# Kernel optimization log

Hardware: AMD Instinct MI355X
Metric: run time of the kernel (lower is better)

The kernel has to match this reference:

```python
import jax, jax.numpy as jnp
import numpy as np

B, D, H, L, T = 4096, 1024, 2048, 256, 8
STD = 0.02


def setup_inputs() -> dict:
    key = jax.random.key(0)
    ks = jax.random.split(key, 24)
    n = lambda k, shp: (jax.random.normal(k, shp, dtype=jnp.float32) * STD)
    inp = {
        "x": jax.random.uniform(ks[0], (B, D), dtype=jnp.float32),
        "task": jax.random.randint(ks[1], (B,), 0, T),
        "eps": jax.random.normal(ks[2], (B, L), dtype=jnp.float32),
        # per-task encoder stacks: in->H->H->H->2L
        "enc_W1": n(ks[3], (T, D, H)), "enc_b1": jnp.zeros((T, H)),
        "enc_W2": n(ks[4], (T, H, H)), "enc_b2": jnp.zeros((T, H)),
        "enc_W3": n(ks[5], (T, H, H)), "enc_b3": jnp.zeros((T, H)),
        "enc_W4": n(ks[6], (T, H, 2 * L)), "enc_b4": jnp.zeros((T, 2 * L)),
        # shared decoder (BayesianLinear means): L->H->H
        "ds_W1": n(ks[7], (L, H)), "ds_b1": jnp.zeros((H,)),
        "ds_W2": n(ks[8], (H, H)), "ds_b2": jnp.zeros((H,)),
        # per-task decoder heads: H->H->D with Sigmoid
        "hd_W1": n(ks[9], (T, H, H)), "hd_b1": jnp.zeros((T, H)),
        "hd_W2": n(ks[10], (T, H, D)), "hd_b2": jnp.zeros((T, D)),
    }
    return inp


def reference(x, task, eps,
              enc_W1, enc_b1, enc_W2, enc_b2, enc_W3, enc_b3, enc_W4, enc_b4,
              ds_W1, ds_b1, ds_W2, ds_b2,
              hd_W1, hd_b1, hd_W2, hd_b2):
    ntasks = enc_W1.shape[0]
    onehot = jax.nn.one_hot(task, ntasks, dtype=x.dtype)  # [B, T], the task==idx mask

    # ---- encode: run every task's encoder on the full batch, mask-sum ----
    def enc_one(W1, b1, W2, b2, W3, b3, W4, b4):
        h = jax.nn.relu(x @ W1 + b1)
        h = jax.nn.relu(h @ W2 + b2)
        h = jax.nn.relu(h @ W3 + b3)
        return h @ W4 + b4  # [B, 2L]

    enc_all = jax.vmap(enc_one)(enc_W1, enc_b1, enc_W2, enc_b2,
                                enc_W3, enc_b3, enc_W4, enc_b4)  # [T, B, 2L]
    scat = jnp.einsum('tbd,bt->bd', enc_all, onehot)  # [B, 2L]
    latent = scat.shape[1] // 2
    mu, log_sigma = scat[:, :latent], scat[:, latent:]
    z = mu + jnp.exp(log_sigma) * eps  # reparameterization

    # ---- decode: shared trunk, then every head masked ----
    h = jax.nn.relu(z @ ds_W1 + ds_b1)
    h = jax.nn.relu(h @ ds_W2 + ds_b2)  # [B, H]

    def head_one(W1, b1, W2, b2):
        g = jax.nn.relu(h @ W1 + b1)
        return jax.nn.sigmoid(g @ W2 + b2)  # [B, D]

    heads_all = jax.vmap(head_one)(hd_W1, hd_b1, hd_W2, hd_b2)  # [T, B, D]
    return jnp.einsum('tbd,bt->bd', heads_all, onehot)  # [B, D]
```

## Files before the change

kernel.cpp:

```cpp
#include <hip/hip_runtime.h>
#include <hip/hip_bf16.h>

#define T_TASKS 8
#define B_ROWS 4096
#define PADROWS 4224
#define BM 128
#define BK 32
#define MAXTILES 40

typedef __attribute__((ext_vector_type(4))) float f32x4;
typedef __attribute__((ext_vector_type(8))) short bf16x8;

#define GLOAD_LDS16(g, l) __builtin_amdgcn_global_load_lds( \
    (const __attribute__((address_space(1))) void*)(g), \
    (__attribute__((address_space(3))) void*)(l), 16, 0, 0)

struct TP { const float* src; unsigned short* dst; int K; int N; int ntiles; };

__device__ __forceinline__ unsigned short f32_to_bf16(float f) {
    union { float f; unsigned int u; } v; v.f = f;
    unsigned int r = v.u + 0x7FFF + ((v.u >> 16) & 1);
    return (unsigned short)(r >> 16);
}

__global__ void setup_kernel(const int* __restrict__ task, int* __restrict__ perm,
                             int* __restrict__ offs, int* __restrict__ table) {
    __shared__ int cnt[T_TASKS];
    __shared__ int cur[T_TASKS];
    int tid = threadIdx.x;
    if (tid < T_TASKS) cnt[tid] = 0;
    __syncthreads();
    for (int b = tid; b < B_ROWS; b += blockDim.x)
        atomicAdd(&cnt[task[b]], 1);
    __syncthreads();
    if (tid == 0) {
        int o = 0;
        for (int t = 0; t < T_TASKS; ++t) { offs[t] = o; cur[t] = o; o += cnt[t]; }
        offs[T_TASKS] = o;
        int s = 0;
        for (int t = 0; t < T_TASKS; ++t) {
            int nt = (cnt[t] + BM - 1) / BM;
            for (int j = 0; j < nt; ++j) table[s++] = (t << 16) | j;
        }
        for (; s < MAXTILES; ++s) table[s] = -1;
    }
    __syncthreads();
    for (int b = tid; b < B_ROWS; b += blockDim.x) {
        int t = task[b];
        int pos = atomicAdd(&cur[t], 1);
        perm[pos] = b;
    }
}

__global__ void permute_cast_kernel(const float* __restrict__ x, const int* __restrict__ perm,
                                    unsigned short* __restrict__ xp) {
    int rowp = blockIdx.x;
    int src = perm[rowp];
    const float4* xin = reinterpret_cast<const float4*>(x + (size_t)src * 1024);
    unsigned short* dst = xp + (size_t)rowp * 1024;
    int c4 = threadIdx.x;
    float4 v = xin[c4];
    ushort4 o;
    o.x = f32_to_bf16(v.x); o.y = f32_to_bf16(v.y);
    o.z = f32_to_bf16(v.z); o.w = f32_to_bf16(v.w);
    *reinterpret_cast<ushort4*>(dst + c4 * 4) = o;
}

__global__ void vae_kernel(const float* __restrict__ scat, const float* __restrict__ eps,
                           const int* __restrict__ perm, unsigned short* __restrict__ z) {
    int rowp = blockIdx.x;
    int c = threadIdx.x;
    int src = perm[rowp];
    float mu = scat[(size_t)rowp * 512 + c];
    float ls = scat[(size_t)rowp * 512 + 256 + c];
    float e  = eps[(size_t)src * 256 + c];
    z[(size_t)rowp * 256 + c] = f32_to_bf16(mu + __expf(ls) * e);
}

__global__ __launch_bounds__(256)
void transpose_cast_kernel(const float* __restrict__ W, unsigned short* __restrict__ Wt,
                           int K, int N) {
    const size_t toff = (size_t)blockIdx.z * K * N;
    const float* Ws = W + toff;
    unsigned short* Wd = Wt + toff;
    const int k0 = blockIdx.x * 64;
    const int n0 = blockIdx.y * 64;
    __shared__ unsigned short Tt[64 * 64];
    const int tid = threadIdx.x;
    const int n = tid & 63;
    const int kq = tid >> 6;
    #pragma unroll
    for (int i = 0; i < 4; ++i) {
        int kk = kq * 16 + i * 4;
        const float* p = Ws + (size_t)(k0 + kk) * N + n0 + n;
        float v0 = p[0];
        float v1 = p[(size_t)N];
        float v2 = p[(size_t)2 * N];
        float v3 = p[(size_t)3 * N];
        unsigned int lo = (unsigned int)f32_to_bf16(v0) | ((unsigned int)f32_to_bf16(v1) << 16);
        unsigned int hi = (unsigned int)f32_to_bf16(v2) | ((unsigned int)f32_to_bf16(v3) << 16);
        int c = (kk >> 2) ^ (n & 15);
        *reinterpret_cast<uint2*>(Tt + n * 64 + c * 4) = make_uint2(lo, hi);
    }
    __syncthreads();
    #pragma unroll
    for (int it = 0; it < 2; ++it) {
        int c  = it * 256 + tid;
        int nn = c >> 3;
        int cg = c & 7;
        int c1 = (cg * 2) ^ (nn & 15);
        int c2 = (cg * 2 + 1) ^ (nn & 15);
        uint2 a = *reinterpret_cast<const uint2*>(Tt + nn * 64 + c1 * 4);
        uint2 b = *reinterpret_cast<const uint2*>(Tt + nn * 64 + c2 * 4);
        uint4 o = make_uint4(a.x, a.y, b.x, b.y);
        *reinterpret_cast<uint4*>(Wd + (size_t)(n0 + nn) * K + k0 + cg * 8) = o;
    }
}

template<int MODE, int BN>
__global__ __launch_bounds__(256, (BN == 64 ? 6 : 4))
void gemm12_kernel(const unsigned short* __restrict__ A,
                   const unsigned short* __restrict__ Wt,
                   const float* __restrict__ bias, void* __restrict__ dst,
                   const int* __restrict__ offs, const int* __restrict__ table,
                   const int* __restrict__ perm,
                   int K, int N, int ldd, int Btot, int GX, TP tpa, TP tpb)
{
    constexpr int NR = BN / 32;
    __shared__ unsigned short As[2][BM * BK];
    __shared__ unsigned short Bs[2][BN * BK];

    const int bxh = blockIdx.x;
    const int tid = threadIdx.x;

    if (bxh >= GX) {
        int tile = (bxh - GX) * gridDim.y + blockIdx.y;
        const float* src; unsigned short* dstp; int tK, tN;
        if (tile < tpa.ntiles) { src = tpa.src; dstp = tpa.dst; tK = tpa.K; tN = tpa.N; }
        else {
            tile -= tpa.ntiles;
            if (tile >= tpb.ntiles) return;
            src = tpb.src; dstp = tpb.dst; tK = tpb.K; tN = tpb.N;
        }
        int tk = tK >> 6, tn = tN >> 6;
        int z = tile / (tk * tn);
        int r = tile % (tk * tn);
        int k0 = (r % tk) * 64, n0 = (r / tk) * 64;
        const size_t toff = (size_t)z * tK * tN;
        const float* Ws = src + toff;
        unsigned short* Wd = dstp + toff;
        unsigned short* Tt = &As[0][0];
        const int n = tid & 63;
        const int kq = tid >> 6;
        #pragma unroll
        for (int i = 0; i < 4; ++i) {
            int kk = kq * 16 + i * 4;
            const float* p = Ws + (size_t)(k0 + kk) * tN + n0 + n;
            float v0 = p[0];
            float v1 = p[(size_t)tN];
            float v2 = p[(size_t)2 * tN];
            float v3 = p[(size_t)3 * tN];
            unsigned int lo = (unsigned int)f32_to_bf16(v0) | ((unsigned int)f32_to_bf16(v1) << 16);
            unsigned int hi = (unsigned int)f32_to_bf16(v2) | ((unsigned int)f32_to_bf16(v3) << 16);
            int c = (kk >> 2) ^ (n & 15);
            *reinterpret_cast<uint2*>(Tt + n * 64 + c * 4) = make_uint2(lo, hi);
        }
        __syncthreads();
        #pragma unroll
        for (int it = 0; it < 2; ++it) {
            int c  = it * 256 + tid;
            int nn = c >> 3;
            int cg = c & 7;
            int c1 = (cg * 2) ^ (nn & 15);
            int c2 = (cg * 2 + 1) ^ (nn & 15);
            uint2 a = *reinterpret_cast<const uint2*>(Tt + nn * 64 + c1 * 4);
            uint2 b = *reinterpret_cast<const uint2*>(Tt + nn * 64 + c2 * 4);
            uint4 o = make_uint4(a.x, a.y, b.x, b.y);
            *reinterpret_cast<uint4*>(Wd + (size_t)(n0 + nn) * tK + k0 + cg * 8) = o;
        }
        return;
    }

    int bx = (bxh & 7) * (GX >> 3) + (bxh >> 3);

    int t, mtile, off, cnt;
    if (table != nullptr) {
        int v = table[bx];
        if (v < 0) return;
        t = v >> 16; mtile = v & 0xFFFF;
        off = offs[t]; cnt = offs[t + 1] - off;
    } else {
        t = 0; mtile = bx; off = 0; cnt = Btot;
    }
    const int n0 = blockIdx.y * BN;

    const int lane = tid & 63;
    const int wave = tid >> 6;
    const int wr = wave >> 1, wc = wave & 1;

    const int rl   = lane >> 2;
    const int csrc = ((lane & 3) ^ ((rl >> 1) & 3)) * 8;
    const unsigned short* Ab = A + ((size_t)(off + mtile * BM + rl)) * K + csrc;
    const unsigned short* Bb = Wt + ((size_t)t * N + n0 + rl) * K + csrc;

    auto stage = [&](int buf, int k0) {
        #pragma unroll
        for (int jj = 0; jj < 2; ++jj) {
            int j = wave * 2 + jj;
            GLOAD_LDS16(Ab + (size_t)(j * 16) * K + k0, &As[buf][j * 512]);
        }
        #pragma unroll
        for (int jb = 0; jb < BN / 64; ++jb) {
            int j = wave * (BN / 64) + jb;
            GLOAD_LDS16(Bb + (size_t)(j * 16) * K + k0, &Bs[buf][j * 512]);
        }
    };

    f32x4 acc[4][NR];
    #pragma unroll
    for (int m = 0; m < 4; ++m)
        #pragma unroll
        for (int n = 0; n < NR; ++n)
            acc[m][n] = (f32x4){0.f, 0.f, 0.f, 0.f};

    auto compute = [&](int buf) {
        bf16x8 af[4], bfr[NR];
        #pragma unroll
        for (int m = 0; m < 4; ++m) {
            int rf = wr * 64 + m * 16 + (lane & 15);
            af[m] = *reinterpret_cast<const bf16x8*>(
                &As[buf][rf * 32 + (((lane >> 4) ^ ((rf >> 1) & 3)) * 8)]);
        }
        #pragma unroll
        for (int n = 0; n < NR; ++n) {
            int nf = wc * (BN / 2) + n * 16 + (lane & 15);
            bfr[n] = *reinterpret_cast<const bf16x8*>(
                &Bs[buf][nf * 32 + (((lane >> 4) ^ ((nf >> 1) & 3)) * 8)]);
        }
        #pragma unroll
        for (int m = 0; m < 4; ++m)
            #pragma unroll
            for (int n = 0; n < NR; ++n)
                acc[m][n] = __builtin_amdgcn_mfma_f32_16x16x32_bf16(af[m], bfr[n], acc[m][n], 0, 0, 0);
    };

    const int nsteps = K / BK;
    stage(0, 0);
    __syncthreads();
    int cur = 0;
    for (int s = 0; s < nsteps; ++s) {
        if (s + 1 < nsteps) stage(cur ^ 1, (s + 1) * BK);
        compute(cur);
        __syncthreads();
        cur ^= 1;
    }

    const float* bt = bias + (size_t)t * N;
    #pragma unroll
    for (int n = 0; n < NR; ++n) {
        int col = n0 + wc * (BN / 2) + n * 16 + (lane & 15);
        float bv = bt[col];
        #pragma unroll
        for (int m = 0; m < 4; ++m) {
            int rbase = mtile * BM + wr * 64 + m * 16 + ((lane >> 4) << 2);
            #pragma unroll
            for (int j = 0; j < 4; ++j) {
                int local = rbase + j;
                if (local >= cnt) continue;
                float v = acc[m][n][j] + bv;
                if (MODE == 0) {
                    ((unsigned short*)dst)[(size_t)(off + local) * ldd + col] =
                        f32_to_bf16(fmaxf(v, 0.f));
                } else if (MODE == 1) {
                    ((float*)dst)[(size_t)(off + local) * ldd + col] = v;
                } else {
                    int grow = perm[off + local];
                    ((float*)dst)[(size_t)grow * ldd + col] = 1.f / (1.f + __expf(-v));
                }
            }
        }
    }
}

extern "C" void kernel_launch(void* const* d_in, const int* in_sizes, int n_in,
                              void* d_out, int out_size, void* d_ws, size_t ws_size,
                              hipStream_t stream) {
    const float* x      = (const float*)d_in[0];
    const int*   task   = (const int*)d_in[1];
    const float* eps    = (const float*)d_in[2];
    const float* enc_W1 = (const float*)d_in[3];
    const float* enc_b1 = (const float*)d_in[4];
    const float* enc_W2 = (const float*)d_in[5];
    const float* enc_b2 = (const float*)d_in[6];
    const float* enc_W3 = (const float*)d_in[7];
    const float* enc_b3 = (const float*)d_in[8];
    const float* enc_W4 = (const float*)d_in[9];
    const float* enc_b4 = (const float*)d_in[10];
    const float* ds_W1  = (const float*)d_in[11];
    const float* ds_b1  = (const float*)d_in[12];
    const float* ds_W2  = (const float*)d_in[13];
    const float* ds_b2  = (const float*)d_in[14];
    const float* hd_W1  = (const float*)d_in[15];
    const float* hd_b1  = (const float*)d_in[16];
    const float* hd_W2  = (const float*)d_in[17];
    const float* hd_b2  = (const float*)d_in[18];
    float* out = (float*)d_out;

    char* ws = (char*)d_ws;
    int* perm  = (int*)ws;
    int* offs  = (int*)(ws + 16384);
    int* table = (int*)(ws + 16384 + 256);
    char* p = ws + 32768;
    unsigned short* xp = (unsigned short*)p; p += (size_t)PADROWS * 1024 * 2;
    unsigned short* h1 = (unsigned short*)p; p += (size_t)PADROWS * 2048 * 2;
    unsigned short* h2 = (unsigned short*)p; p += (size_t)PADROWS * 2048 * 2;
    unsigned short* zb = (unsigned short*)p; p += (size_t)PADROWS * 256 * 2;
    unsigned short* tw1  = (unsigned short*)p; p += (size_t)8 * 2048 * 1024 * 2;
    unsigned short* tw2  = (unsigned short*)p; p += (size_t)8 * 2048 * 2048 * 2;
    unsigned short* tw3  = (unsigned short*)p; p += (size_t)8 * 2048 * 2048 * 2;
    unsigned short* tw4  = (unsigned short*)p; p += (size_t)8 * 512 * 2048 * 2;
    unsigned short* tds1 = (unsigned short*)p; p += (size_t)2048 * 256 * 2;
    unsigned short* tds2 = (unsigned short*)p; p += (size_t)2048 * 2048 * 2;
    unsigned short* thd1 = (unsigned short*)p; p += (size_t)8 * 2048 * 2048 * 2;
    unsigned short* thd2 = (unsigned short*)p; p += (size_t)8 * 1024 * 2048 * 2;
    float* scat = out;

    const TP tnone = { nullptr, nullptr, 64, 64, 0 };
    const TP tpW2  = { enc_W2, tw2, 2048, 2048, 8192 };
    const TP tpW3  = { enc_W3, tw3, 2048, 2048, 8192 };
    const TP tpW4  = { enc_W4, tw4, 2048,  512, 2048 };
    const TP tpDS1 = { ds_W1, tds1,  256, 2048,  128 };
    const TP tpDS2 = { ds_W2, tds2, 2048, 2048, 1024 };
    const TP tpHD1 = { hd_W1, thd1, 2048, 2048, 8192 };
    const TP tpHD2 = { hd_W2, thd2, 2048, 1024, 4096 };

    setup_kernel<<<1, 1024, 0, stream>>>(task, perm, offs, table);
    permute_cast_kernel<<<B_ROWS, 256, 0, stream>>>(x, perm, xp);

    transpose_cast_kernel<<<dim3(16, 32, 8), 256, 0, stream>>>(enc_W1, tw1, 1024, 2048);

    gemm12_kernel<0, 128><<<dim3(552, 16), 256, 0, stream>>>(xp, tw1, enc_b1, h1, offs, table, nullptr, 1024, 2048, 2048, B_ROWS, MAXTILES, tpW2, tnone);
    gemm12_kernel<0, 128><<<dim3(552, 16), 256, 0, stream>>>(h1, tw2, enc_b2, h2, offs, table, nullptr, 2048, 2048, 2048, B_ROWS, MAXTILES, tpW3, tnone);
    gemm12_kernel<0, 128><<<dim3(176, 16), 256, 0, stream>>>(h2, tw3, enc_b3, h1, offs, table, nullptr, 2048, 2048, 2048, B_ROWS, MAXTILES, tpW4, tpDS1);
    gemm12_kernel<1, 64><<<dim3(168, 8), 256, 0, stream>>>(h1, tw4, enc_b4, scat, offs, table, nullptr, 2048, 512, 512, B_ROWS, MAXTILES, tpDS2, tnone);

    vae_kernel<<<B_ROWS, 256, 0, stream>>>(scat, eps, perm, zb);

    gemm12_kernel<0, 128><<<dim3(544, 16), 256, 0, stream>>>(zb, tds1, ds_b1, h2, nullptr, nullptr, nullptr, 256, 2048, 2048, B_ROWS, 32, tpHD1, tnone);
    gemm12_kernel<0, 128><<<dim3(288, 16), 256, 0, stream>>>(h2, tds2, ds_b2, h1, nullptr, nullptr, nullptr, 2048, 2048, 2048, B_ROWS, 32, tpHD2, tnone);

    gemm12_kernel<0, 128><<<dim3(MAXTILES, 16), 256, 0, stream>>>(h1, thd1, hd_b1, h2, offs, table, nullptr, 2048, 2048, 2048, B_ROWS, MAXTILES, tnone, tnone);
    gemm12_kernel<2, 64><<<dim3(MAXTILES, 16), 256, 0, stream>>>(h2, thd2, hd_b2, out, offs, table, perm, 2048, 1024, 1024, B_ROWS, MAXTILES, tnone, tnone);
}
```

Measured before the change: 618.0 us.

## Add 256x256 8-wave ping-pong GEMM kernel for large H×H layers

After: 726.8 us. +17.6%, slower.

```diff
diff --git a/kernel.cpp b/kernel.cpp
--- a/kernel.cpp
+++ b/kernel.cpp
@@ -3,10 +3,9 @@
 
 #define T_TASKS 8
 #define B_ROWS 4096
-#define PADROWS 4224
-#define BM 128
-#define BK 32
-#define MAXTILES 40
+#define PADROWS 4352
+#define MAXT128 40
+#define MAXT256 24
 
 typedef __attribute__((ext_vector_type(4))) float f32x4;
 typedef __attribute__((ext_vector_type(8))) short bf16x8;
@@ -14,6 +13,9 @@
 #define GLOAD_LDS16(g, l) __builtin_amdgcn_global_load_lds( \
     (const __attribute__((address_space(1))) void*)(g), \
     (__attribute__((address_space(3))) void*)(l), 16, 0, 0)
+
+#define WAITV2() asm volatile("s_waitcnt vmcnt(2)" ::: "memory")
+#define PBAR()   asm volatile("s_barrier" ::: "memory")
 
 struct TP { const float* src; unsigned short* dst; int K; int N; int ntiles; };
 
@@ -24,7 +26,8 @@
 }
 
 __global__ void setup_kernel(const int* __restrict__ task, int* __restrict__ perm,
-                             int* __restrict__ offs, int* __restrict__ table) {
+                             int* __restrict__ offs, int* __restrict__ table128,
+                             int* __restrict__ table256) {
     __shared__ int cnt[T_TASKS];
     __shared__ int cur[T_TASKS];
     int tid = threadIdx.x;
@@ -39,10 +42,16 @@
         offs[T_TASKS] = o;
         int s = 0;
         for (int t = 0; t < T_TASKS; ++t) {
-            int nt = (cnt[t] + BM - 1) / BM;
-            for (int j = 0; j < nt; ++j) table[s++] = (t << 16) | j;
-        }
-        for (; s < MAXTILES; ++s) table[s] = -1;
+            int nt = (cnt[t] + 127) >> 7;
+            for (int j = 0; j < nt; ++j) table128[s++] = (t << 16) | j;
+        }
+        for (; s < MAXT128; ++s) table128[s] = -1;
+        s = 0;
+        for (int t = 0; t < T_TASKS; ++t) {
+            int nt = (cnt[t] + 255) >> 8;
+            for (int j = 0; j < nt; ++j) table256[s++] = (t << 16) | j;
+        }
+        for (; s < MAXT256; ++s) table256[s] = -1;
     }
     __syncthreads();
     for (int b = tid; b < B_ROWS; b += blockDim.x) {
@@ -117,6 +126,191 @@
     }
 }
 
+template<int MODE>
+__global__ __launch_bounds__(512, 2)
+void gemm8p_kernel(const unsigned short* __restrict__ A,
+                   const unsigned short* __restrict__ Wt,
+                   const float* __restrict__ bias, void* __restrict__ dst,
+                   const int* __restrict__ offs, const int* __restrict__ table,
+                   const int* __restrict__ perm,
+                   int K, int N, int ldd, int Btot, int GX, TP tpa, TP tpb)
+{
+    __shared__ unsigned short As_[2][256 * 64];
+    __shared__ unsigned short Bs_[2][256 * 64];
+
+    const int bxh = blockIdx.x;
+    const int tid = threadIdx.x;
+
+    if (bxh >= GX) {
+        int half = tid >> 8;
+        int ltid = tid & 255;
+        int tile = ((bxh - GX) * gridDim.y + blockIdx.y) * 2 + half;
+        unsigned short* Tt = &As_[0][0] + half * 4096;
+        const float* src = nullptr; unsigned short* dstp = nullptr; int tK = 64, tN = 64;
+        bool act = true;
+        if (tile < tpa.ntiles) { src = tpa.src; dstp = tpa.dst; tK = tpa.K; tN = tpa.N; }
+        else {
+            tile -= tpa.ntiles;
+            if (tile >= tpb.ntiles) act = false;
+            else { src = tpb.src; dstp = tpb.dst; tK = tpb.K; tN = tpb.N; }
+        }
+        int k0 = 0, n0 = 0; size_t toff = 0;
+        if (act) {
+            int tk = tK >> 6, tn = tN >> 6;
+            int z = tile / (tk * tn);
+            int r = tile % (tk * tn);
+            k0 = (r % tk) * 64; n0 = (r / tk) * 64;
+            toff = (size_t)z * tK * tN;
+        }
+        const int n = ltid & 63;
+        const int kq = ltid >> 6;
+        if (act) {
+            const float* Ws = src + toff;
+            #pragma unroll
+            for (int i = 0; i < 4; ++i) {
+                int kk = kq * 16 + i * 4;
+                const float* p = Ws + (size_t)(k0 + kk) * tN + n0 + n;
+                float v0 = p[0];
+                float v1 = p[(size_t)tN];
+                float v2 = p[(size_t)2 * tN];
+                float v3 = p[(size_t)3 * tN];
+                unsigned int lo = (unsigned int)f32_to_bf16(v0) | ((unsigned int)f32_to_bf16(v1) << 16);
+                unsigned int hi = (unsigned int)f32_to_bf16(v2) | ((unsigned int)f32_to_bf16(v3) << 16);
+                int c = (kk >> 2) ^ (n & 15);
+                *reinterpret_cast<uint2*>(Tt + n * 64 + c * 4) = make_uint2(lo, hi);
+            }
+        }
+        __syncthreads();
+        if (act) {
+            unsigned short* Wd = dstp + toff;
+            #pragma unroll
+            for (int it = 0; it < 2; ++it) {
+                int c  = it * 256 + ltid;
+                int nn = c >> 3;
+                int cg = c & 7;
+                int c1 = (cg * 2) ^ (nn & 15);
+                int c2 = (cg * 2 + 1) ^ (nn & 15);
+                uint2 a = *reinterpret_cast<const uint2*>(Tt + nn * 64 + c1 * 4);
+                uint2 b = *reinterpret_cast<const uint2*>(Tt + nn * 64 + c2 * 4);
+                uint4 o = make_uint4(a.x, a.y, b.x, b.y);
+                *reinterpret_cast<uint4*>(Wd + (size_t)(n0 + nn) * tK + k0 + cg * 8) = o;
+            }
+        }
+        return;
+    }
+
+    int bx = (bxh & 7) * (GX >> 3) + (bxh >> 3);
+
+    int t, mtile, off, cnt;
+    if (table != nullptr) {
+        int v = table[bx];
+        if (v < 0) return;
+        t = v >> 16; mtile = v & 0xFFFF;
+        off = offs[t]; cnt = offs[t + 1] - off;
+    } else {
+        t = 0; mtile = bx; off = 0; cnt = Btot;
+    }
+    const int n0 = blockIdx.y * 256;
+
+    const int lane = tid & 63;
+    const int wave = tid >> 6;
+    const int wm = wave >> 2;
+    const int wn = wave & 3;
+
+    const int aRow  = lane >> 3;
+    const int aSlot = ((lane & 7) ^ aRow) * 8;
+    const unsigned short* Ab = A + ((size_t)(off + mtile * 256 + aRow)) * K + aSlot;
+    const unsigned short* Bb = Wt + ((size_t)t * N + n0 + aRow) * K + aSlot;
+
+    const int nt = K >> 6;
+
+    auto stA = [&](int c, int h, int kt) {
+        int k0 = (kt < nt ? kt : nt - 1) << 6;
+        #pragma unroll
+        for (int j = 0; j < 2; ++j) {
+            int r0 = h * 128 + (wave * 2 + j) * 8;
+            GLOAD_LDS16(Ab + (size_t)r0 * K + k0, &As_[c][r0 * 64]);
+        }
+    };
+    auto stB = [&](int c, int h, int kt) {
+        int k0 = (kt < nt ? kt : nt - 1) << 6;
+        #pragma unroll
+        for (int j = 0; j < 2; ++j) {
+            int r0 = h * 128 + (wave * 2 + j) * 8;
+            GLOAD_LDS16(Bb + (size_t)r0 * K + k0, &Bs_[c][r0 * 64]);
+        }
+    };
+
+    f32x4 acc[8][4];
+    #pragma unroll
+    for (int m = 0; m < 8; ++m)
+        #pragma unroll
+        for (int n = 0; n < 4; ++n)
+            acc[m][n] = (f32x4){0.f, 0.f, 0.f, 0.f};
+
+    auto comp = [&](int c, int mg, int kf) {
+        bf16x8 af[4], bfr[4];
+        #pragma unroll
+        for (int m = 0; m < 4; ++m) {
+            int rf = wm * 128 + (mg * 4 + m) * 16 + (lane & 15);
+            af[m] = *reinterpret_cast<const bf16x8*>(
+                &As_[c][rf * 64 + (((kf * 4 + (lane >> 4)) ^ (rf & 7)) * 8)]);
+        }
+        #pragma unroll
+        for (int n = 0; n < 4; ++n) {
+            int nf = wn * 64 + n * 16 + (lane & 15);
+            bfr[n] = *reinterpret_cast<const bf16x8*>(
+                &Bs_[c][nf * 64 + (((kf * 4 + (lane >> 4)) ^ (nf & 7)) * 8)]);
+        }
+        #pragma unroll
+        for (int m = 0; m < 4; ++m)
+            #pragma unroll
+            for (int n = 0; n < 4; ++n)
+                acc[mg * 4 + m][n] =
+                    __builtin_amdgcn_mfma_f32_16x16x32_bf16(af[m], bfr[n], acc[mg * 4 + m][n], 0, 0, 0);
+    };
+
+    stB(0, 0, 0); stB(0, 1, 0); stA(0, 0, 0); stA(0, 1, 0);
+
+    for (int i = 0; i < (nt >> 1); ++i) {
+        int T1 = 2 * i + 1, T2 = 2 * i + 2;
+        stB(1, 0, T1); WAITV2(); PBAR(); comp(0, 0, 0); PBAR();
+        stB(1, 1, T1);           PBAR(); comp(0, 1, 0); PBAR();
+        stA(1, 0, T1);           PBAR(); comp(0, 0, 1); PBAR();
+        stA(1, 1, T1);           PBAR(); comp(0, 1, 1); PBAR();
+        stB(0, 0, T2); WAITV2(); PBAR(); comp(1, 0, 0); PBAR();
+        stB(0, 1, T2);           PBAR(); comp(1, 1, 0); PBAR();
+        stA(0, 0, T2);           PBAR(); comp(1, 0, 1); PBAR();
+        stA(0, 1, T2);           PBAR(); comp(1, 1, 1); PBAR();
+    }
+
+    const float* bt = bias + (size_t)t * N;
+    #pragma unroll
+    for (int mi = 0; mi < 8; ++mi) {
+        int rbase = mtile * 256 + wm * 128 + mi * 16 + ((lane >> 4) << 2);
+        #pragma unroll
+        for (int n = 0; n < 4; ++n) {
+            int col = n0 + wn * 64 + n * 16 + (lane & 15);
+            float bv = bt[col];
+            #pragma unroll
+            for (int j = 0; j < 4; ++j) {
+                int local = rbase + j;
+                if (local >= cnt) continue;
+                float v = acc[mi][n][j] + bv;
+                if (MODE == 0) {
+                    ((unsigned short*)dst)[(size_t)(off + local) * ldd + col] =
+                        f32_to_bf16(fmaxf(v, 0.f));
+                } else if (MODE == 1) {
+                    ((float*)dst)[(size_t)(off + local) * ldd + col] = v;
+                } else {
+                    int grow = perm[off + local];
+                    ((float*)dst)[(size_t)grow * ldd + col] = 1.f / (1.f + __expf(-v));
+                }
+            }
+        }
+    }
+}
+
 template<int MODE, int BN>
 __global__ __launch_bounds__(256, (BN == 64 ? 6 : 4))
 void gemm12_kernel(const unsigned short* __restrict__ A,
@@ -126,6 +320,7 @@
                    const int* __restrict__ perm,
                    int K, int N, int ldd, int Btot, int GX, TP tpa, TP tpb)
 {
+    constexpr int BM = 128, BK = 32;
     constexpr int NR = BN / 32;
     __shared__ unsigned short As[2][BM * BK];
     __shared__ unsigned short Bs[2][BN * BK];
@@ -307,9 +502,10 @@
     float* out = (float*)d_out;
 
     char* ws = (char*)d_ws;
-    int* perm  = (int*)ws;
-    int* offs  = (int*)(ws + 16384);
-    int* table = (int*)(ws + 16384 + 256);
+    int* perm     = (int*)ws;
+    int* offs     = (int*)(ws + 16384);
+    int* table128 = (int*)(ws + 16384 + 256);
+    int* table256 = (int*)(ws + 16384 + 512);
     char* p = ws + 32768;
     unsigned short* xp = (unsigned short*)p; p += (size_t)PADROWS * 1024 * 2;
     unsigned short* h1 = (unsigned short*)p; p += (size_t)PADROWS * 2048 * 2;
@@ -334,21 +530,21 @@
     const TP tpHD1 = { hd_W1, thd1, 2048, 2048, 8192 };
     const TP tpHD2 = { hd_W2, thd2, 2048, 1024, 4096 };
 
-    setup_kernel<<<1, 1024, 0, stream>>>(task, perm, offs, table);
+    setup_kernel<<<1, 1024, 0, stream>>>(task, perm, offs, table128, table256);
     permute_cast_kernel<<<B_ROWS, 256, 0, stream>>>(x, perm, xp);
 
     transpose_cast_kernel<<<dim3(16, 32, 8), 256, 0, stream>>>(enc_W1, tw1, 1024, 2048);
 
-    gemm12_kernel<0, 128><<<dim3(552, 16), 256, 0, stream>>>(xp, tw1, enc_b1, h1, offs, table, nullptr, 1024, 2048, 2048, B_ROWS, MAXTILES, tpW2, tnone);
-    gemm12_kernel<0, 128><<<dim3(552, 16), 256, 0, stream>>>(h1, tw2, enc_b2, h2, offs, table, nullptr, 2048, 2048, 2048, B_ROWS, MAXTILES, tpW3, tnone);
-    gemm12_kernel<0, 128><<<dim3(176, 16), 256, 0, stream>>>(h2, tw3, enc_b3, h1, offs, table, nullptr, 2048, 2048, 2048, B_ROWS, MAXTILES, tpW4, tpDS1);
-    gemm12_kernel<1, 64><<<dim3(168, 8), 256, 0, stream>>>(h1, tw4, enc_b4, scat, offs, table, nullptr, 2048, 512, 512, B_ROWS, MAXTILES, tpDS2, tnone);
+    gemm8p_kernel<0><<<dim3(536, 8), 512, 0, stream>>>(xp, tw1, enc_b1, h1, offs, table256, nullptr, 1024, 2048, 2048, B_ROWS, MAXT256, tpW2, tnone);
+    gemm8p_kernel<0><<<dim3(536, 8), 512, 0, stream>>>(h1, tw2, enc_b2, h2, offs, table256, nullptr, 2048, 2048, 2048, B_ROWS, MAXT256, tpW3, tnone);
+    gemm8p_kernel<0><<<dim3(160, 8), 512, 0, stream>>>(h2, tw3, enc_b3, h1, offs, table256, nullptr, 2048, 2048, 2048, B_ROWS, MAXT256, tpW4, tpDS1);
+    gemm12_kernel<1, 64><<<dim3(168, 8), 256, 0, stream>>>(h1, tw4, enc_b4, scat, offs, table128, nullptr, 2048, 512, 512, B_ROWS, MAXT128, tpDS2, tnone);
 
     vae_kernel<<<B_ROWS, 256, 0, stream>>>(scat, eps, perm, zb);
 
     gemm12_kernel<0, 128><<<dim3(544, 16), 256, 0, stream>>>(zb, tds1, ds_b1, h2, nullptr, nullptr, nullptr, 256, 2048, 2048, B_ROWS, 32, tpHD1, tnone);
-    gemm12_kernel<0, 128><<<dim3(288, 16), 256, 0, stream>>>(h2, tds2, ds_b2, h1, nullptr, nullptr, nullptr, 2048, 2048, 2048, B_ROWS, 32, tpHD2, tnone);
-
-    gemm12_kernel<0, 128><<<dim3(MAXTILES, 16), 256, 0, stream>>>(h1, thd1, hd_b1, h2, offs, table, nullptr, 2048, 2048, 2048, B_ROWS, MAXTILES, tnone, tnone);
-    gemm12_kernel<2, 64><<<dim3(MAXTILES, 16), 256, 0, stream>>>(h2, thd2, hd_b2, out, offs, table, perm, 2048, 1024, 1024, B_ROWS, MAXTILES, tnone, tnone);
-}
+    gemm8p_kernel<0><<<dim3(272, 8), 512, 0, stream>>>(h2, tds2, ds_b2, h1, nullptr, nullptr, nullptr, 2048, 2048, 2048, B_ROWS, 16, tpHD2, tnone);
+
+    gemm8p_kernel<0><<<dim3(24, 8), 512, 0, stream>>>(h1, thd1, hd_b1, h2, offs, table256, nullptr, 2048, 2048, 2048, B_ROWS, MAXT256, tnone, tnone);
+    gemm12_kernel<2, 64><<<dim3(MAXT128, 16), 256, 0, stream>>>(h2, thd2, hd_b2, out, offs, table128, perm, 2048, 1024, 1024, B_ROWS, MAXT128, tnone, tnone);
+}
```
